# Kernel optimization log

Hardware: AMD Instinct MI355X
Metric: run time of the kernel (lower is better)

Reference implementation:

```python
import jax, jax.numpy as jnp
import numpy as np

B, N, F = 4, 3000, 128

def setup_inputs() -> dict:
    key = jax.random.key(0)
    k1, k2, k3, k4 = jax.random.split(key, 4)
    x = jax.random.normal(k1, (B, N, F), dtype=jnp.float32)
    adj = jax.random.uniform(k2, (B, N, N), dtype=jnp.float32)
    h0 = jax.random.normal(k3, (B, N, F), dtype=jnp.float32)
    stdv = 1.0 / np.sqrt(F)
    theta = jax.random.uniform(k4, (F, F), dtype=jnp.float32, minval=-stdv, maxval=stdv)
    return {
        "x": x, "adj": adj, "h0": h0, "theta": theta,
        "lamda": jnp.float32(0.5), "alpha": jnp.float32(0.1), "l": 4,
    }

def _normalize_adj(adj):
    # add self loops, then D^{-1/2} A D^{-1/2} via elementwise row/col scaling
    # (same math as diag-embed + inverse + two bmms in the original)
    n = adj.shape[1]
    adj = adj + jnp.eye(n, dtype=adj.dtype)
    deg = jnp.sum(adj, axis=2)                      # [B, N]
    d_inv_sqrt = jax.lax.rsqrt(deg)                 # [B, N]
    return d_inv_sqrt[:, :, None] * adj * d_inv_sqrt[:, None, :]

def reference(x, adj, h0, theta, lamda, alpha, l):
    adj_n = _normalize_adj(adj)
    beta = jnp.log(lamda / l + 1.0)
    hi = jnp.einsum('bnm,bmf->bnf', adj_n, x)       # aggregation
    support = (1.0 - alpha) * hi + alpha * h0       # variant=False path
    r = support
    out = beta * jnp.einsum('bnf,fg->bng', support, theta) + (1.0 - beta) * r
    return out
```

## Files before the change

### kernel.cpp

```cpp
#include <hip/hip_runtime.h>
#include <hip/hip_bf16.h>
#include <math.h>

#define BB 4
#define NN 3000
#define FF 128
#define NKC 94
#define NIT 188

typedef __bf16 bf16x8 __attribute__((ext_vector_type(8)));
typedef float  f32x4  __attribute__((ext_vector_type(4)));

__global__ __launch_bounds__(256) void k_degpack(const float* __restrict__ adj,
                                                 __bf16* __restrict__ apk,
                                                 float* __restrict__ dis) {
    __shared__ float tile[16][260];
    const int b  = blockIdx.y;
    const int it = blockIdx.x;
    const int i0 = it * 16;
    const int t  = threadIdx.x, w = t >> 6, l = t & 63;
    const int m  = l & 15, quad = l >> 4;
    float dreg[4] = {0.f, 0.f, 0.f, 0.f};
    __bf16* dst = apk + ((size_t)(b * NIT + it) * NKC) * 512 + l * 8;
    for (int c = 0; c < 12; ++c) {
        int k0 = c * 256;
        #pragma unroll
        for (int i = 0; i < 4; ++i) {
            int row = i * 4 + w;
            int col = k0 + l * 4;
            float4 v = {0.f, 0.f, 0.f, 0.f};
            if (i0 + row < NN && col < NN)
                v = *(const float4*)(adj + ((size_t)b * NN + i0 + row) * NN + col);
            dreg[i] += (v.x + v.y) + (v.z + v.w);
            *(float4*)&tile[row][l * 4] = v;
        }
        __syncthreads();
        int nk = (c == 11) ? 6 : 8;
        #pragma unroll
        for (int h = 0; h < 2; ++h) {
            int kcl = w + h * 4;
            if (kcl < nk) {
                bf16x8 a;
                #pragma unroll
                for (int j = 0; j < 8; ++j)
                    a[j] = (__bf16)tile[m][kcl * 32 + quad * 8 + j];
                *(bf16x8*)(dst + (size_t)(c * 8 + kcl) * 512) = a;
            }
        }
        __syncthreads();
    }
    #pragma unroll
    for (int i = 0; i < 4; ++i) {
        float s = dreg[i];
        for (int off = 32; off > 0; off >>= 1) s += __shfl_down(s, off, 64);
        int irow = i0 + i * 4 + w;
        if (l == 0 && irow < NN) dis[b * NN + irow] = 1.0f / sqrtf(s + 1.0f);
    }
}

__global__ __launch_bounds__(256) void k_xpk(const float* __restrict__ x,
                                             const float* __restrict__ dis,
                                             __bf16* __restrict__ xpk) {
    int b  = blockIdx.y, kc = blockIdx.x;
    int t  = threadIdx.x, w = t >> 6, l = t & 63;
    int m  = l & 15, q = l >> 4;
    #pragma unroll
    for (int h = 0; h < 2; ++h) {
        int nt = w + h * 4;
        int f  = nt * 16 + m;
        bf16x8 v;
        #pragma unroll
        for (int j = 0; j < 8; ++j) {
            int k = kc * 32 + q * 8 + j;
            float val = 0.f;
            if (k < NN) val = dis[b * NN + k] * x[((size_t)b * NN + k) * FF + f];
            v[j] = (__bf16)val;
        }
        *(bf16x8*)(xpk + ((size_t)(b * 8 + nt) * NKC + kc) * 512 + l * 8) = v;
    }
}

__global__ __launch_bounds__(256) void k_thpk(const float* __restrict__ theta,
                                              __bf16* __restrict__ thpk) {
    int kc = blockIdx.x;
    int t  = threadIdx.x, w = t >> 6, l = t & 63;
    int m  = l & 15, q = l >> 4;
    #pragma unroll
    for (int h = 0; h < 2; ++h) {
        int nt = w + h * 4;
        bf16x8 v;
        #pragma unroll
        for (int j = 0; j < 8; ++j) {
            int k = kc * 32 + q * 8 + j;
            v[j] = (__bf16)theta[k * FF + nt * 16 + m];
        }
        *(bf16x8*)(thpk + ((size_t)(nt * 4 + kc)) * 512 + l * 8) = v;
    }
}

__global__ __launch_bounds__(256) void k_agg(const __bf16* __restrict__ apk,
                                             const __bf16* __restrict__ xpk,
                                             const __bf16* __restrict__ thpk,
                                             const float* __restrict__ x,
                                             const float* __restrict__ h0,
                                             const float* __restrict__ dis,
                                             float* __restrict__ out,
                                             const float* __restrict__ alpha_p,
                                             const float* __restrict__ lamda_p,
                                             const int* __restrict__ l_p) {
    __shared__ __bf16 stile[16][136];
    const int b  = blockIdx.y;
    const int it = blockIdx.x;
    const int i0 = it * 16;
    const int t  = threadIdx.x, w = t >> 6, l = t & 63;
    const int m  = l & 15, quad = l >> 4;
    const int n0 = w * 32;
    const __bf16* Ap = apk + ((size_t)(b * NIT + it) * NKC) * 512 + l * 8;
    const __bf16* B0 = xpk + ((size_t)(b * 8 + 2 * w) * NKC) * 512 + l * 8;
    const __bf16* B1 = B0 + (size_t)NKC * 512;
    f32x4 acc0 = {0.f, 0.f, 0.f, 0.f};
    f32x4 acc1 = {0.f, 0.f, 0.f, 0.f};
    #pragma unroll 2
    for (int kc = 0; kc < NKC; ++kc) {
        bf16x8 a  = *(const bf16x8*)(Ap + (size_t)kc * 512);
        bf16x8 b0 = *(const bf16x8*)(B0 + (size_t)kc * 512);
        bf16x8 b1 = *(const bf16x8*)(B1 + (size_t)kc * 512);
        acc0 = __builtin_amdgcn_mfma_f32_16x16x32_bf16(a, b0, acc0, 0, 0, 0);
        acc1 = __builtin_amdgcn_mfma_f32_16x16x32_bf16(a, b1, acc1, 0, 0, 0);
    }
    const float alpha = *alpha_p;
    const float beta  = logf(*lamda_p / (float)(*l_p) + 1.0f);
    float s0v[4], s1v[4];
    #pragma unroll
    for (int r = 0; r < 4; ++r) {
        int row  = quad * 4 + r;
        int irow = i0 + row;
        float s0 = 0.f, s1 = 0.f;
        if (irow < NN) {
            float  di   = dis[b * NN + irow];
            size_t base = ((size_t)b * NN + irow) * FF;
            int c0 = n0 + m, c1 = n0 + 16 + m;
            s0 = (1.f - alpha) * (di * acc0[r] + di * di * x[base + c0]) + alpha * h0[base + c0];
            s1 = (1.f - alpha) * (di * acc1[r] + di * di * x[base + c1]) + alpha * h0[base + c1];
        }
        s0v[r] = s0; s1v[r] = s1;
        stile[row][n0 + m]      = (__bf16)s0;
        stile[row][n0 + 16 + m] = (__bf16)s1;
    }
    __syncthreads();
    f32x4 o0 = {0.f, 0.f, 0.f, 0.f};
    f32x4 o1 = {0.f, 0.f, 0.f, 0.f};
    const __bf16* T0 = thpk + (size_t)(2 * w * 4) * 512 + l * 8;
    const __bf16* T1 = T0 + 4 * 512;
    #pragma unroll
    for (int kc = 0; kc < 4; ++kc) {
        bf16x8 a   = *(const bf16x8*)&stile[m][kc * 32 + quad * 8];
        bf16x8 tb0 = *(const bf16x8*)(T0 + (size_t)kc * 512);
        bf16x8 tb1 = *(const bf16x8*)(T1 + (size_t)kc * 512);
        o0 = __builtin_amdgcn_mfma_f32_16x16x32_bf16(a, tb0, o0, 0, 0, 0);
        o1 = __builtin_amdgcn_mfma_f32_16x16x32_bf16(a, tb1, o1, 0, 0, 0);
    }
    const float omb = 1.f - beta;
    #pragma unroll
    for (int r = 0; r < 4; ++r) {
        int irow = i0 + quad * 4 + r;
        if (irow < NN) {
            size_t base = ((size_t)b * NN + irow) * FF;
            out[base + n0 + m]      = beta * o0[r] + omb * s0v[r];
            out[base + n0 + 16 + m] = beta * o1[r] + omb * s1v[r];
        }
    }
}

extern "C" void kernel_launch(void* const* d_in, const int* in_sizes, int n_in,
                              void* d_out, int out_size, void* d_ws, size_t ws_size,
                              hipStream_t stream) {
    const float* x      = (const float*)d_in[0];
    const float* adj    = (const float*)d_in[1];
    const float* h0     = (const float*)d_in[2];
    const float* theta  = (const float*)d_in[3];
    const float* lamda  = (const float*)d_in[4];
    const float* alpha  = (const float*)d_in[5];
    const int*   l      = (const int*)d_in[6];
    float* out = (float*)d_out;

    char*   ws   = (char*)d_ws;
    float*  dis  = (float*)ws;
    __bf16* xpk  = (__bf16*)(ws + 65536);
    __bf16* thpk = (__bf16*)(ws + 3200000);
    __bf16* apk  = (__bf16*)(ws + 4 * 1024 * 1024);

    k_degpack<<<dim3(NIT, BB), 256, 0, stream>>>(adj, apk, dis);
    k_thpk<<<dim3(4), 256, 0, stream>>>(theta, thpk);
    k_xpk<<<dim3(NKC, BB), 256, 0, stream>>>(x, dis, xpk);
    k_agg<<<dim3(NIT, BB), 256, 0, stream>>>(apk, xpk, thpk, x, h0, dis, out,
                                             alpha, lamda, l);
}
```

Before: 287.3 us.

## Repack adjacency via ds_bpermute with per-wave half-row split and atomic degree

The adjacency pack kernel drops the LDS tile and the block barriers. Each wave now handles half of a 16-row strip, reading 8 consecutive floats per lane, converting them to bf16 and rearranging them into MFMA fragment layout with ds_bpermute. Row degrees are built from partial sums with atomicAdd into a buffer that is zeroed by a memset first. The rsqrt is moved into the consumer kernels, and the aggregation loop unroll goes from 2 to 4. In exchange the change adds an extra memset launch, atomics, and recomputation of the rsqrt in the consumers.

Result: slower. 315.3 us (+9.7%).

```diff
diff --git a/kernel.cpp b/kernel.cpp
--- a/kernel.cpp
+++ b/kernel.cpp
@@ -13,53 +13,49 @@
 
 __global__ __launch_bounds__(256) void k_degpack(const float* __restrict__ adj,
                                                  __bf16* __restrict__ apk,
-                                                 float* __restrict__ dis) {
-    __shared__ float tile[16][260];
-    const int b  = blockIdx.y;
-    const int it = blockIdx.x;
-    const int i0 = it * 16;
-    const int t  = threadIdx.x, w = t >> 6, l = t & 63;
-    const int m  = l & 15, quad = l >> 4;
-    float dreg[4] = {0.f, 0.f, 0.f, 0.f};
+                                                 float* __restrict__ deg) {
+    const int b    = blockIdx.y;
+    const int gw   = blockIdx.x * 4 + (threadIdx.x >> 6);
+    const int it   = gw >> 1;
+    const int half = gw & 1;
+    const int l    = threadIdx.x & 63;
+    const int srow = l >> 2, scb = l & 3;
+    const int m    = l & 15, quad = l >> 4;
+    const int i0   = it * 16;
+    const int irow = i0 + srow;
+    const bool rowok = irow < NN;
+    const float* rp = adj + ((size_t)b * NN + (rowok ? irow : 0)) * NN;
     __bf16* dst = apk + ((size_t)(b * NIT + it) * NKC) * 512 + l * 8;
-    for (int c = 0; c < 12; ++c) {
-        int k0 = c * 256;
+    const int addr = (m * 4 + quad) * 4;
+    float rs = 0.f;
+    const int kc0 = half * 47, kc1 = kc0 + 47;
+    #pragma unroll 4
+    for (int kc = kc0; kc < kc1; ++kc) {
+        int col = kc * 32 + scb * 8;
+        float4 u = {0.f, 0.f, 0.f, 0.f}, v = {0.f, 0.f, 0.f, 0.f};
+        if (rowok && col < NN) {
+            u = *(const float4*)(rp + col);
+            v = *(const float4*)(rp + col + 4);
+        }
+        rs += ((u.x + u.y) + (u.z + u.w)) + ((v.x + v.y) + (v.z + v.w));
+        union { __bf16 h[8]; int d[4]; } P;
+        P.h[0] = (__bf16)u.x; P.h[1] = (__bf16)u.y;
+        P.h[2] = (__bf16)u.z; P.h[3] = (__bf16)u.w;
+        P.h[4] = (__bf16)v.x; P.h[5] = (__bf16)v.y;
+        P.h[6] = (__bf16)v.z; P.h[7] = (__bf16)v.w;
+        union { int d[4]; bf16x8 f; } Q;
         #pragma unroll
-        for (int i = 0; i < 4; ++i) {
-            int row = i * 4 + w;
-            int col = k0 + l * 4;
-            float4 v = {0.f, 0.f, 0.f, 0.f};
-            if (i0 + row < NN && col < NN)
-                v = *(const float4*)(adj + ((size_t)b * NN + i0 + row) * NN + col);
-            dreg[i] += (v.x + v.y) + (v.z + v.w);
-            *(float4*)&tile[row][l * 4] = v;
-        }
-        __syncthreads();
-        int nk = (c == 11) ? 6 : 8;
-        #pragma unroll
-        for (int h = 0; h < 2; ++h) {
-            int kcl = w + h * 4;
-            if (kcl < nk) {
-                bf16x8 a;
-                #pragma unroll
-                for (int j = 0; j < 8; ++j)
-                    a[j] = (__bf16)tile[m][kcl * 32 + quad * 8 + j];
-                *(bf16x8*)(dst + (size_t)(c * 8 + kcl) * 512) = a;
-            }
-        }
-        __syncthreads();
+        for (int t2 = 0; t2 < 4; ++t2)
+            Q.d[t2] = __builtin_amdgcn_ds_bpermute(addr, P.d[t2]);
+        *(bf16x8*)(dst + (size_t)kc * 512) = Q.f;
     }
-    #pragma unroll
-    for (int i = 0; i < 4; ++i) {
-        float s = dreg[i];
-        for (int off = 32; off > 0; off >>= 1) s += __shfl_down(s, off, 64);
-        int irow = i0 + i * 4 + w;
-        if (l == 0 && irow < NN) dis[b * NN + irow] = 1.0f / sqrtf(s + 1.0f);
-    }
+    rs += __shfl_down(rs, 2, 64);
+    rs += __shfl_down(rs, 1, 64);
+    if ((l & 3) == 0 && rowok) atomicAdd(&deg[b * NN + irow], rs);
 }
 
 __global__ __launch_bounds__(256) void k_xpk(const float* __restrict__ x,
-                                             const float* __restrict__ dis,
+                                             const float* __restrict__ deg,
                                              __bf16* __restrict__ xpk) {
     int b  = blockIdx.y, kc = blockIdx.x;
     int t  = threadIdx.x, w = t >> 6, l = t & 63;
@@ -73,7 +69,10 @@
         for (int j = 0; j < 8; ++j) {
             int k = kc * 32 + q * 8 + j;
             float val = 0.f;
-            if (k < NN) val = dis[b * NN + k] * x[((size_t)b * NN + k) * FF + f];
+            if (k < NN) {
+                float di = 1.0f / sqrtf(deg[b * NN + k] + 1.0f);
+                val = di * x[((size_t)b * NN + k) * FF + f];
+            }
             v[j] = (__bf16)val;
         }
         *(bf16x8*)(xpk + ((size_t)(b * 8 + nt) * NKC + kc) * 512 + l * 8) = v;
@@ -103,7 +102,7 @@
                                              const __bf16* __restrict__ thpk,
                                              const float* __restrict__ x,
                                              const float* __restrict__ h0,
-                                             const float* __restrict__ dis,
+                                             const float* __restrict__ deg,
                                              float* __restrict__ out,
                                              const float* __restrict__ alpha_p,
                                              const float* __restrict__ lamda_p,
@@ -120,7 +119,7 @@
     const __bf16* B1 = B0 + (size_t)NKC * 512;
     f32x4 acc0 = {0.f, 0.f, 0.f, 0.f};
     f32x4 acc1 = {0.f, 0.f, 0.f, 0.f};
-    #pragma unroll 2
+    #pragma unroll 4
     for (int kc = 0; kc < NKC; ++kc) {
         bf16x8 a  = *(const bf16x8*)(Ap + (size_t)kc * 512);
         bf16x8 b0 = *(const bf16x8*)(B0 + (size_t)kc * 512);
@@ -137,7 +136,7 @@
         int irow = i0 + row;
         float s0 = 0.f, s1 = 0.f;
         if (irow < NN) {
-            float  di   = dis[b * NN + irow];
+            float  di   = 1.0f / sqrtf(deg[b * NN + irow] + 1.0f);
             size_t base = ((size_t)b * NN + irow) * FF;
             int c0 = n0 + m, c1 = n0 + 16 + m;
             s0 = (1.f - alpha) * (di * acc0[r] + di * di * x[base + c0]) + alpha * h0[base + c0];
@@ -185,14 +184,15 @@
     float* out = (float*)d_out;
 
     char*   ws   = (char*)d_ws;
-    float*  dis  = (float*)ws;
+    float*  deg  = (float*)ws;
     __bf16* xpk  = (__bf16*)(ws + 65536);
     __bf16* thpk = (__bf16*)(ws + 3200000);
     __bf16* apk  = (__bf16*)(ws + 4 * 1024 * 1024);
 
-    k_degpack<<<dim3(NIT, BB), 256, 0, stream>>>(adj, apk, dis);
+    hipMemsetAsync(deg, 0, BB * NN * sizeof(float), stream);
+    k_degpack<<<dim3(94, BB), 256, 0, stream>>>(adj, apk, deg);
     k_thpk<<<dim3(4), 256, 0, stream>>>(theta, thpk);
-    k_xpk<<<dim3(NKC, BB), 256, 0, stream>>>(x, dis, xpk);
-    k_agg<<<dim3(NIT, BB), 256, 0, stream>>>(apk, xpk, thpk, x, h0, dis, out,
+    k_xpk<<<dim3(NKC, BB), 256, 0, stream>>>(x, deg, xpk);
+    k_agg<<<dim3(NIT, BB), 256, 0, stream>>>(apk, xpk, thpk, x, h0, deg, out,
                                              alpha, lamda, l);
 }
```
